# Optimization experiments

Hardware: AMD Instinct MI355X
Metric: run time of the kernel (lower is better)

## Reference

```python
import jax, jax.numpy as jnp
import numpy as np

B, V, H, W, CIN, COUT = 2, 4, 256, 256, 64, 64
WINDOW = 1
GAMMA = 0.1


def setup_inputs() -> dict:
    key = jax.random.key(0)
    ks = jax.random.split(key, 6)
    # gaussian positions: x,y in [-1,1], z in [0.5,2.5] so projection masks are nontrivial
    means = jax.random.uniform(ks[0], (B, V, H, W, 3), dtype=jnp.float32)
    means = means * jnp.array([2.0, 2.0, 2.0], jnp.float32) + jnp.array([-1.0, -1.0, 0.5], jnp.float32)
    depths = jax.random.uniform(ks[1], (B, V, H, W, 1, 1), dtype=jnp.float32)
    gs_feats = jax.random.normal(ks[2], (B, V, H, W, CIN), dtype=jnp.float32)
    # normalized intrinsics (ndc in [0,1))
    intr = jnp.array([[0.8, 0.0, 0.5], [0.0, 0.8, 0.5], [0.0, 0.0, 1.0]], jnp.float32)
    intrinsics = jnp.broadcast_to(intr, (B, V, 3, 3))
    # camera-to-world extrinsics: identity rotation, small per-view translations
    t = jax.random.uniform(ks[3], (B, V, 3), minval=-0.2, maxval=0.2, dtype=jnp.float32)
    extrinsics = jnp.broadcast_to(jnp.eye(4, dtype=jnp.float32), (B, V, 4, 4)).at[..., :3, 3].set(t)
    w1 = jax.random.normal(ks[4], (COUT, CIN, 3, 3), dtype=jnp.float32) * 0.05
    b1 = jnp.zeros((COUT,), jnp.float32)
    w2 = jax.random.normal(ks[5], (COUT, COUT, 3, 3), dtype=jnp.float32) * 0.05
    b2 = jnp.zeros((COUT,), jnp.float32)
    return {"means": means, "depths": depths, "gs_feats": gs_feats,
            "intrinsics": intrinsics, "extrinsics": extrinsics,
            "w1": w1, "b1": b1, "w2": w2, "b2": b2}


def _project(points, intr, extr, eps=1e-8):
    # points (b, n, 3) world; extr (b,4,4) cam-to-world; intr (b,3,3) normalized
    w2c = jnp.linalg.inv(extr)
    ph = jnp.concatenate([points, jnp.ones_like(points[..., :1])], axis=-1)  # (b,n,4)
    cam = jnp.einsum('bij,bnj->bni', w2c, ph)[..., :3]
    z = cam[..., 2:3]
    ndc = jnp.einsum('bij,bnj->bni', intr, cam / (z + eps))
    return ndc[..., :2], cam[..., 2] > eps


def _conv3x3(x, w, b):
    y = jax.lax.conv_general_dilated(x, w, (1, 1), 'SAME',
                                     dimension_numbers=('NCHW', 'OIHW', 'NCHW'))
    return y + b[None, :, None, None]


def reference(means, depths, gs_feats, intrinsics, extrinsics, w1, b1, w2, b2):
    b, v, h, w_, c = gs_feats.shape
    hw = h * w_
    feats_flat = gs_feats.reshape(b, v, hw, c)
    pts = means.reshape(b, v, hw, 3)
    outs = []
    for j in range(v):
        acc = feats_flat[:, j]                      # (b, hw, c)
        norm = jnp.ones((b,), gs_feats.dtype)
        for k in range(v):
            if j != k and (k - WINDOW) <= j <= (k + WINDOW):
                ndc, valid_z = _project(pts[:, j], intrinsics[:, k], extrinsics[:, k])
                px = jnp.floor(ndc[..., 0] * w_).astype(jnp.int32)
                py = jnp.floor(ndc[..., 1] * h).astype(jnp.int32)
                mask = ((ndc[..., 0] >= 0) & (ndc[..., 0] < 1) &
                        (ndc[..., 1] >= 0) & (ndc[..., 1] < 1) & valid_z)  # (b,hw)
                idx = jnp.clip(py, 0, h - 1) * w_ + jnp.clip(px, 0, w_ - 1)
                gathered = jnp.take_along_axis(feats_flat[:, k], idx[..., None], axis=1)
                upd = jnp.where(mask[..., None], gathered, jnp.zeros((), gs_feats.dtype))
                scale = GAMMA * mask.sum(-1).astype(gs_feats.dtype) / (h * w_)  # (b,)
                acc = acc + upd * scale[:, None, None]
                norm = norm + scale
        outs.append(acc / norm[:, None, None])
    fused = jnp.stack(outs, axis=1).reshape(b * v, h, w_, c).transpose(0, 3, 1, 2)  # (bv,c,h,w)
    x = _conv3x3(fused, w1, b1)
    x = jax.nn.gelu(x, approximate=False)
    x = _conv3x3(x, w2, b2)
    return x.transpose(0, 2, 3, 1).reshape(b, v, h, w_, -1)
```

## Files before the change

kernel.cpp:

```cpp
#include <hip/hip_runtime.h>
#include <math.h>

#define HW 65536
#define NPAD 258

typedef short bf16x8 __attribute__((ext_vector_type(8)));
typedef float f32x4  __attribute__((ext_vector_type(4)));

#define O_COUNTS 0
#define O_W2C    2048
#define O_WT     4096
#define O_META   151552
#define O_FUSED  3297280
#define O_X1     71458816

#define HROWB   4224
#define HROWSTR 4240
#define HBUFB   (6 * HROWSTR)

__device__ __forceinline__ unsigned short f2bf(float f) {
    unsigned int u = __float_as_uint(f);
    u += 0x7FFFu + ((u >> 16) & 1u);
    return (unsigned short)(u >> 16);
}

__device__ __forceinline__ float gelu_fast(float v) {
    float x  = v * 0.70710678118654752f;
    float ax = fabsf(x);
    float t  = __builtin_amdgcn_rcpf(fmaf(0.3275911f, ax, 1.0f));
    float p  = fmaf(t, 1.061405429f, -1.453152027f);
    p = fmaf(t, p, 1.421413741f);
    p = fmaf(t, p, -0.284496736f);
    p = fmaf(t, p, 0.254829592f);
    p = p * t;
    float e   = __expf(-x * x);
    float era = fmaf(-p, e, 1.0f);
    float er  = copysignf(era, x);
    return 0.5f * v * (1.0f + er);
}

__global__ __launch_bounds__(256) void prep_kernel(
    const float* __restrict__ extr, const float* __restrict__ w1,
    const float* __restrict__ w2, float* __restrict__ w2c,
    unsigned short* __restrict__ wT, unsigned short* __restrict__ fusedP,
    unsigned short* __restrict__ x1P, int* __restrict__ counts)
{
    int tid = blockIdx.x * blockDim.x + threadIdx.x;
    int nth = gridDim.x * blockDim.x;

    if (blockIdx.x == 0) {
        if (threadIdx.x < 8) {
            float a[4][8];
            const float* E = extr + threadIdx.x * 16;
            for (int r = 0; r < 4; r++)
                for (int c = 0; c < 4; c++) {
                    a[r][c] = E[r*4 + c];
                    a[r][4+c] = (r == c) ? 1.0f : 0.0f;
                }
            for (int col = 0; col < 4; col++) {
                int piv = col; float bm = fabsf(a[col][col]);
                for (int r = col+1; r < 4; r++) {
                    float v = fabsf(a[r][col]);
                    if (v > bm) { bm = v; piv = r; }
                }
                if (piv != col)
                    for (int c = 0; c < 8; c++) { float t = a[col][c]; a[col][c] = a[piv][c]; a[piv][c] = t; }
                float f = 1.0f / a[col][col];
                for (int c = 0; c < 8; c++) a[col][c] *= f;
                for (int r = 0; r < 4; r++) if (r != col) {
                    float f2 = a[r][col];
                    for (int c = 0; c < 8; c++) a[r][c] -= f2 * a[col][c];
                }
            }
            float* O = w2c + threadIdx.x * 16;
            for (int r = 0; r < 4; r++)
                for (int c = 0; c < 4; c++) O[r*4+c] = a[r][4+c];
        }
    }

    for (int i = tid; i < 384; i += nth) counts[i] = 0;

    for (int e = tid; e < 73728; e += nth) {
        int t = e;
        int j  = t & 7;  t >>= 3;
        int co = t & 63; t >>= 6;
        int q  = t & 3;  t >>= 2;
        int tap = t % 9; t /= 9;
        int h  = t & 1;  int cv = t >> 1;
        int ci = h*32 + q*8 + j;
        int ky = tap / 3, kx = tap % 3;
        const float* wsrc = cv ? w2 : w1;
        float v = wsrc[((co*64 + ci)*3 + ky)*3 + kx];
        wT[cv*36864 + ((((h*9 + tap)*4 + q)*64 + co)*8 + j)] = f2bf(v);
    }

    for (int u = tid; u < 2*8*1028*8; u += nth) {
        int t = u;
        int ch   = t & 7;    t >>= 3;
        int cell = t % 1028; t /= 1028;
        int n    = t & 7;    int buf = t >> 3;
        int y, x;
        if      (cell < 258) { y = 0;   x = cell; }
        else if (cell < 516) { y = 257; x = cell - 258; }
        else if (cell < 772) { y = cell - 516 + 1; x = 0; }
        else                 { y = cell - 772 + 1; x = 257; }
        unsigned short* p = (buf ? x1P : fusedP) +
            (((size_t)(n*NPAD + y)*NPAD + x)*64 + ch*8);
        *reinterpret_cast<uint4*>(p) = make_uint4(0u, 0u, 0u, 0u);
    }
}

__global__ __launch_bounds__(256) void proj_kernel(
    const float* __restrict__ means, const float* __restrict__ intr,
    const float* __restrict__ w2c, int* __restrict__ meta,
    int* __restrict__ counts)
{
    const int jt[6] = {0,1,1,2,2,3};
    const int kt[6] = {1,0,2,1,3,2};
    int s = blockIdx.y;
    int b = s / 6, p = s % 6;
    int j = jt[p], k = kt[p];
    int i = blockIdx.x * 256 + threadIdx.x;

    __shared__ int bcnt;
    if (threadIdx.x == 0) bcnt = 0;
    __syncthreads();

    const float* mp = means + ((size_t)(b*4 + j)*HW + i)*3;
    float x = mp[0], y = mp[1], z = mp[2];
    const float* M = w2c + (b*4 + k)*16;
    const float* I = intr + (b*4 + k)*9;

    float cx = fmaf(M[2],  z, fmaf(M[1], y, M[0]*x)) + M[3];
    float cy = fmaf(M[6],  z, fmaf(M[5], y, M[4]*x)) + M[7];
    float cz = fmaf(M[10], z, fmaf(M[9], y, M[8]*x)) + M[11];

    bool vz = cz > 1e-8f;
    float zi = cz + 1e-8f;
    float sx = cx / zi, sy = cy / zi, sz = cz / zi;
    float nx = fmaf(I[2], sz, fmaf(I[1], sy, I[0]*sx));
    float ny = fmaf(I[5], sz, fmaf(I[4], sy, I[3]*sx));

    int px = (int)floorf(nx * 256.0f);
    int py = (int)floorf(ny * 256.0f);
    bool mask = (nx >= 0.0f) && (nx < 1.0f) && (ny >= 0.0f) && (ny < 1.0f) && vz;
    int pxc = min(max(px, 0), 255);
    int pyc = min(max(py, 0), 255);
    int idx = pyc*256 + pxc;
    meta[(size_t)s*HW + i] = idx | (mask ? (int)0x80000000 : 0);

    unsigned long long bal = __ballot(mask ? 1 : 0);
    if ((threadIdx.x & 63) == 0)
        atomicAdd(&bcnt, (int)__popcll(bal));
    __syncthreads();
    if (threadIdx.x == 0)
        atomicAdd(counts + s*32, bcnt);
}

__global__ __launch_bounds__(256) void fuse_kernel(
    const float* __restrict__ feats, const int* __restrict__ meta,
    const int* __restrict__ counts, unsigned short* __restrict__ fusedP)
{
    const int nsl[4]    = {1, 2, 2, 1};
    const int slt[4][2] = {{0,0},{1,2},{3,4},{5,5}};
    const int kvw[4][2] = {{1,1},{0,2},{1,3},{2,2}};

    int bj = blockIdx.y;
    int b = bj >> 2, j = bj & 3;
    int pt = blockIdx.x * 16 + (threadIdx.x >> 4);
    int cg = threadIdx.x & 15;

    const float4* fj = reinterpret_cast<const float4*>(
        feats + ((size_t)bj*HW + pt)*64) + cg;
    float4 acc = *fj;
    float norm = 1.0f;
    int ns = nsl[j];
    for (int e = 0; e < 2; e++) {
        if (e < ns) {
            int p = slt[j][e], k = kvw[j][e];
            int s = b*6 + p;
            float scale = 0.1f * (float)counts[s*32] / 65536.0f;
            int mt = meta[(size_t)s*HW + pt];
            if (mt < 0) {
                int idx = mt & 0xFFFF;
                const float4* g = reinterpret_cast<const float4*>(
                    feats + ((size_t)(b*4 + k)*HW + idx)*64) + cg;
                float4 gv = *g;
                acc.x += scale * gv.x; acc.y += scale * gv.y;
                acc.z += scale * gv.z; acc.w += scale * gv.w;
            }
            norm += scale;
        }
    }
    float ox = acc.x / norm, oy = acc.y / norm;
    float oz = acc.z / norm, ow = acc.w / norm;

    int yy = pt >> 8, xx = pt & 255;
    unsigned short* op = fusedP +
        (((size_t)bj*NPAD + (yy+1))*NPAD + (xx+1))*64 + cg*4;
    ushort4 o = make_ushort4(f2bf(ox), f2bf(oy), f2bf(oz), f2bf(ow));
    *reinterpret_cast<ushort4*>(op) = o;
}

template<int MODE>
__global__ __launch_bounds__(256) void conv_kernel(
    const unsigned short* __restrict__ in, const unsigned short* __restrict__ wT,
    const float* __restrict__ bias, void* __restrict__ outp)
{
    __shared__ unsigned short smem[2 * HBUFB / 2];

    int n = blockIdx.z;
    int Y0 = blockIdx.y * 8;
    int X0 = blockIdx.x * 64;
    int w  = threadIdx.x >> 6;
    int lane = threadIdx.x & 63;
    int m = lane & 15, q = lane >> 4;

    int srcl = ((lane >> 2) * 128) + ((((lane & 3) ^ ((lane >> 3) & 3)) & 3) << 4);
    int tsrcl = 8192 + ((lane >> 2) * 128) + ((lane & 3) << 4);

    int vb[3];
#pragma unroll
    for (int dx = 0; dx < 3; dx++)
        vb[dx] = w*HROWSTR + m*64 + (((q ^ (((m + dx) >> 1) & 3)) & 3) << 4);

    const char* gin = (const char*)in;

    auto STAGE = [&](int t, int h, int buf) {
        const char* gb = gin + (((size_t)(n*NPAD) + (size_t)(Y0 + 4*t)) * NPAD + X0) * 128 + h*64;
        char* lb = (char*)smem + buf*HBUFB;
        for (int ri = w; ri < 6; ri += 4) {
            const char* g = gb + (size_t)ri * (NPAD*128);
            char* l = lb + ri*HROWSTR;
#pragma unroll
            for (int i = 0; i < 4; i++)
                __builtin_amdgcn_global_load_lds(
                    (const __attribute__((address_space(1))) unsigned int*)(g + i*2048 + srcl),
                    (__attribute__((address_space(3))) unsigned int*)(l + i*1024 + (size_t)lane*16),
                    16, 0, 0);
            if (lane < 8)
                __builtin_amdgcn_global_load_lds(
                    (const __attribute__((address_space(1))) unsigned int*)(g + tsrcl),
                    (__attribute__((address_space(3))) unsigned int*)(l + 4096 + (size_t)lane*16),
                    16, 0, 0);
        }
    };

    f32x4 acc[4][4];
    auto ACCZERO = [&]() {
#pragma unroll
        for (int a = 0; a < 4; a++)
#pragma unroll
            for (int bq = 0; bq < 4; bq++)
                acc[a][bq] = (f32x4){0.f, 0.f, 0.f, 0.f};
    };

    auto COMPUTE = [&](int h, int buf) {
        const char* sb = (const char*)smem + buf*HBUFB;
        const char* wb = (const char*)wT + h*9*4096 + q*1024 + m*16;
#pragma unroll
        for (int tap = 0; tap < 9; tap++) {
            int dy = tap/3, dx = tap%3;
            bf16x8 av[4], bv[4];
#pragma unroll
            for (int Mt = 0; Mt < 4; Mt++)
                av[Mt] = *reinterpret_cast<const bf16x8*>(
                    sb + vb[dx] + dy*HROWSTR + Mt*1024 + dx*64);
#pragma unroll
            for (int Nt = 0; Nt < 4; Nt++)
                bv[Nt] = *reinterpret_cast<const bf16x8*>(wb + tap*4096 + Nt*256);
#pragma unroll
            for (int Mt = 0; Mt < 4; Mt++)
#pragma unroll
                for (int Nt = 0; Nt < 4; Nt++)
                    acc[Mt][Nt] = __builtin_amdgcn_mfma_f32_16x16x32_bf16(
                        bv[Nt], av[Mt], acc[Mt][Nt], 0, 0, 0);
        }
    };

    float4 bsv[4];
#pragma unroll
    for (int Nt = 0; Nt < 4; Nt++)
        bsv[Nt] = *reinterpret_cast<const float4*>(bias + Nt*16 + q*4);

    auto EPI = [&](int t) {
        int yout = Y0 + 4*t + w;
#pragma unroll
        for (int Mt = 0; Mt < 4; Mt++) {
            int px = X0 + Mt*16 + m;
#pragma unroll
            for (int Nt = 0; Nt < 4; Nt++) {
                int co0 = Nt*16 + q*4;
                float v0 = acc[Mt][Nt][0] + bsv[Nt].x;
                float v1 = acc[Mt][Nt][1] + bsv[Nt].y;
                float v2 = acc[Mt][Nt][2] + bsv[Nt].z;
                float v3 = acc[Mt][Nt][3] + bsv[Nt].w;
                if (MODE == 1) {
                    v0 = gelu_fast(v0); v1 = gelu_fast(v1);
                    v2 = gelu_fast(v2); v3 = gelu_fast(v3);
                    unsigned short* o = (unsigned short*)outp +
                        ((size_t)(n*NPAD + yout + 1)*NPAD + (px + 1))*64 + co0;
                    ushort4 pk = make_ushort4(f2bf(v0), f2bf(v1), f2bf(v2), f2bf(v3));
                    *reinterpret_cast<ushort4*>(o) = pk;
                } else {
                    float* o = (float*)outp +
                        ((size_t)(n*256 + yout)*256 + px)*64 + co0;
                    *reinterpret_cast<float4*>(o) = make_float4(v0, v1, v2, v3);
                }
            }
        }
    };

    STAGE(0, 0, 0);
    __syncthreads();

    STAGE(0, 1, 1);
    ACCZERO();
    COMPUTE(0, 0);
    __syncthreads();

    STAGE(1, 0, 0);
    COMPUTE(1, 1);
    __syncthreads();

    STAGE(1, 1, 1);
    EPI(0);
    ACCZERO();
    COMPUTE(0, 0);
    __syncthreads();

    COMPUTE(1, 1);
    EPI(1);
}

extern "C" void kernel_launch(void* const* d_in, const int* in_sizes, int n_in,
                              void* d_out, int out_size, void* d_ws, size_t ws_size,
                              hipStream_t stream)
{
    const float* means = (const float*)d_in[0];
    const float* feats = (const float*)d_in[2];
    const float* intr  = (const float*)d_in[3];
    const float* extr  = (const float*)d_in[4];
    const float* w1    = (const float*)d_in[5];
    const float* b1    = (const float*)d_in[6];
    const float* w2    = (const float*)d_in[7];
    const float* b2    = (const float*)d_in[8];

    char* ws = (char*)d_ws;
    int*            counts = (int*)(ws + O_COUNTS);
    float*          w2c    = (float*)(ws + O_W2C);
    unsigned short* wT     = (unsigned short*)(ws + O_WT);
    int*            meta   = (int*)(ws + O_META);
    unsigned short* fusedP = (unsigned short*)(ws + O_FUSED);
    unsigned short* x1P    = (unsigned short*)(ws + O_X1);

    prep_kernel<<<dim3(96), dim3(256), 0, stream>>>(
        extr, w1, w2, w2c, wT, fusedP, x1P, counts);
    proj_kernel<<<dim3(256, 12), dim3(256), 0, stream>>>(
        means, intr, w2c, meta, counts);
    fuse_kernel<<<dim3(4096, 8), dim3(256), 0, stream>>>(
        feats, meta, counts, fusedP);
    conv_kernel<1><<<dim3(4, 32, 8), dim3(256), 0, stream>>>(
        fusedP, wT, b1, (void*)x1P);
    conv_kernel<2><<<dim3(4, 32, 8), dim3(256), 0, stream>>>(
        x1P, wT + 36864, b2, d_out);
}
```

Before: 419.2 us.

## Shrink conv tiles to four rows, single-buffer LDS, raise occupancy

```diff
diff --git a/kernel.cpp b/kernel.cpp
--- a/kernel.cpp
+++ b/kernel.cpp
@@ -203,14 +203,14 @@
 }
 
 template<int MODE>
-__global__ __launch_bounds__(256) void conv_kernel(
+__global__ __launch_bounds__(256, 6) void conv_kernel(
     const unsigned short* __restrict__ in, const unsigned short* __restrict__ wT,
     const float* __restrict__ bias, void* __restrict__ outp)
 {
-    __shared__ unsigned short smem[2 * HBUFB / 2];
+    __shared__ unsigned short smem[HBUFB / 2];
 
     int n = blockIdx.z;
-    int Y0 = blockIdx.y * 8;
+    int y0 = blockIdx.y * 4;
     int X0 = blockIdx.x * 64;
     int w  = threadIdx.x >> 6;
     int lane = threadIdx.x & 63;
@@ -224,14 +224,22 @@
     for (int dx = 0; dx < 3; dx++)
         vb[dx] = w*HROWSTR + m*64 + (((q ^ (((m + dx) >> 1) & 3)) & 3) << 4);
 
-    const char* gin = (const char*)in;
-
-    auto STAGE = [&](int t, int h, int buf) {
-        const char* gb = gin + (((size_t)(n*NPAD) + (size_t)(Y0 + 4*t)) * NPAD + X0) * 128 + h*64;
-        char* lb = (char*)smem + buf*HBUFB;
+    f32x4 acc[4][4];
+#pragma unroll
+    for (int a = 0; a < 4; a++)
+#pragma unroll
+        for (int bq = 0; bq < 4; bq++)
+            acc[a][bq] = (f32x4){0.f, 0.f, 0.f, 0.f};
+
+#pragma unroll
+    for (int h = 0; h < 2; h++) {
+        if (h) __syncthreads();
+
+        const char* gb = (const char*)in +
+            (((size_t)(n*NPAD) + y0) * NPAD + X0) * 128 + h*64;
         for (int ri = w; ri < 6; ri += 4) {
             const char* g = gb + (size_t)ri * (NPAD*128);
-            char* l = lb + ri*HROWSTR;
+            char* l = (char*)smem + ri*HROWSTR;
 #pragma unroll
             for (int i = 0; i < 4; i++)
                 __builtin_amdgcn_global_load_lds(
@@ -244,20 +252,9 @@
                     (__attribute__((address_space(3))) unsigned int*)(l + 4096 + (size_t)lane*16),
                     16, 0, 0);
         }
-    };
-
-    f32x4 acc[4][4];
-    auto ACCZERO = [&]() {
-#pragma unroll
-        for (int a = 0; a < 4; a++)
-#pragma unroll
-            for (int bq = 0; bq < 4; bq++)
-                acc[a][bq] = (f32x4){0.f, 0.f, 0.f, 0.f};
-    };
-
-    auto COMPUTE = [&](int h, int buf) {
-        const char* sb = (const char*)smem + buf*HBUFB;
-        const char* wb = (const char*)wT + h*9*4096 + q*1024 + m*16;
+        __syncthreads();
+
+        const char* wb = (const char*)wT + h*36864 + q*1024 + m*16;
 #pragma unroll
         for (int tap = 0; tap < 9; tap++) {
             int dy = tap/3, dx = tap%3;
@@ -265,7 +262,7 @@
 #pragma unroll
             for (int Mt = 0; Mt < 4; Mt++)
                 av[Mt] = *reinterpret_cast<const bf16x8*>(
-                    sb + vb[dx] + dy*HROWSTR + Mt*1024 + dx*64);
+                    (const char*)smem + vb[dx] + dy*HROWSTR + Mt*1024 + dx*64);
 #pragma unroll
             for (int Nt = 0; Nt < 4; Nt++)
                 bv[Nt] = *reinterpret_cast<const bf16x8*>(wb + tap*4096 + Nt*256);
@@ -276,61 +273,34 @@
                     acc[Mt][Nt] = __builtin_amdgcn_mfma_f32_16x16x32_bf16(
                         bv[Nt], av[Mt], acc[Mt][Nt], 0, 0, 0);
         }
-    };
-
-    float4 bsv[4];
-#pragma unroll
-    for (int Nt = 0; Nt < 4; Nt++)
-        bsv[Nt] = *reinterpret_cast<const float4*>(bias + Nt*16 + q*4);
-
-    auto EPI = [&](int t) {
-        int yout = Y0 + 4*t + w;
+    }
+
+    int yout = y0 + w;
+#pragma unroll
+    for (int Nt = 0; Nt < 4; Nt++) {
+        float4 bs = *reinterpret_cast<const float4*>(bias + Nt*16 + q*4);
+        int co0 = Nt*16 + q*4;
 #pragma unroll
         for (int Mt = 0; Mt < 4; Mt++) {
             int px = X0 + Mt*16 + m;
-#pragma unroll
-            for (int Nt = 0; Nt < 4; Nt++) {
-                int co0 = Nt*16 + q*4;
-                float v0 = acc[Mt][Nt][0] + bsv[Nt].x;
-                float v1 = acc[Mt][Nt][1] + bsv[Nt].y;
-                float v2 = acc[Mt][Nt][2] + bsv[Nt].z;
-                float v3 = acc[Mt][Nt][3] + bsv[Nt].w;
-                if (MODE == 1) {
-                    v0 = gelu_fast(v0); v1 = gelu_fast(v1);
-                    v2 = gelu_fast(v2); v3 = gelu_fast(v3);
-                    unsigned short* o = (unsigned short*)outp +
-                        ((size_t)(n*NPAD + yout + 1)*NPAD + (px + 1))*64 + co0;
-                    ushort4 pk = make_ushort4(f2bf(v0), f2bf(v1), f2bf(v2), f2bf(v3));
-                    *reinterpret_cast<ushort4*>(o) = pk;
-                } else {
-                    float* o = (float*)outp +
-                        ((size_t)(n*256 + yout)*256 + px)*64 + co0;
-                    *reinterpret_cast<float4*>(o) = make_float4(v0, v1, v2, v3);
-                }
+            float v0 = acc[Mt][Nt][0] + bs.x;
+            float v1 = acc[Mt][Nt][1] + bs.y;
+            float v2 = acc[Mt][Nt][2] + bs.z;
+            float v3 = acc[Mt][Nt][3] + bs.w;
+            if (MODE == 1) {
+                v0 = gelu_fast(v0); v1 = gelu_fast(v1);
+                v2 = gelu_fast(v2); v3 = gelu_fast(v3);
+                unsigned short* o = (unsigned short*)outp +
+                    ((size_t)(n*NPAD + yout + 1)*NPAD + (px + 1))*64 + co0;
+                ushort4 pk = make_ushort4(f2bf(v0), f2bf(v1), f2bf(v2), f2bf(v3));
+                *reinterpret_cast<ushort4*>(o) = pk;
+            } else {
+                float* o = (float*)outp +
+                    ((size_t)(n*256 + yout)*256 + px)*64 + co0;
+                *reinterpret_cast<float4*>(o) = make_float4(v0, v1, v2, v3);
             }
         }
-    };
-
-    STAGE(0, 0, 0);
-    __syncthreads();
-
-    STAGE(0, 1, 1);
-    ACCZERO();
-    COMPUTE(0, 0);
-    __syncthreads();
-
-    STAGE(1, 0, 0);
-    COMPUTE(1, 1);
-    __syncthreads();
-
-    STAGE(1, 1, 1);
-    EPI(0);
-    ACCZERO();
-    COMPUTE(0, 0);
-    __syncthreads();
-
-    COMPUTE(1, 1);
-    EPI(1);
+    }
 }
 
 extern "C" void kernel_launch(void* const* d_in, const int* in_sizes, int n_in,
@@ -360,8 +330,8 @@
         means, intr, w2c, meta, counts);
     fuse_kernel<<<dim3(4096, 8), dim3(256), 0, stream>>>(
         feats, meta, counts, fusedP);
-    conv_kernel<1><<<dim3(4, 32, 8), dim3(256), 0, stream>>>(
+    conv_kernel<1><<<dim3(4, 64, 8), dim3(256), 0, stream>>>(
         fusedP, wT, b1, (void*)x1P);
-    conv_kernel<2><<<dim3(4, 32, 8), dim3(256), 0, stream>>>(
+    conv_kernel<2><<<dim3(4, 64, 8), dim3(256), 0, stream>>>(
         x1P, wT + 36864, b2, d_out);
 }
```

Result: slower. 821.3 us (+95.9%).
